# Kernel tuning notes

Hardware: AMD Instinct MI355X
Metric: run time of the kernel (lower is better)

Reference implementation:

```python
import jax, jax.numpy as jnp
import numpy as np

B, N, CS, CZ, H, C, PQ, PV = 1, 512, 384, 128, 12, 16, 4, 8
INF, EPS = 1e5, 1e-8


def _quat_to_rot(q):
    # q: [..., 4] unit quaternion -> [..., 3, 3] rotation matrix
    w, x, y, z = q[..., 0], q[..., 1], q[..., 2], q[..., 3]
    r0 = jnp.stack([1 - 2 * (y * y + z * z), 2 * (x * y - w * z), 2 * (x * z + w * y)], -1)
    r1 = jnp.stack([2 * (x * y + w * z), 1 - 2 * (x * x + z * z), 2 * (y * z - w * x)], -1)
    r2 = jnp.stack([2 * (x * z - w * y), 2 * (y * z + w * x), 1 - 2 * (x * x + y * y)], -1)
    return jnp.stack([r0, r1, r2], -2)


def setup_inputs() -> dict:
    key = jax.random.key(0)
    ks = jax.random.split(key, 20)
    sc = 0.02
    quat = jax.random.normal(ks[0], (B, N, 4), jnp.float32)
    quat = quat / jnp.linalg.norm(quat, axis=-1, keepdims=True)
    concat_dim = H * (C + PV * 4 + CZ)
    return {
        "s": jax.random.normal(ks[1], (B, N, CS), jnp.float32),
        "z": jax.random.normal(ks[2], (B, N, N, CZ), jnp.float32),
        "rot": _quat_to_rot(quat),
        "trans": jax.random.normal(ks[3], (B, N, 3), jnp.float32),
        "mask": jnp.ones((B, N), jnp.float32),
        "W_q": jax.random.normal(ks[4], (CS, H * C), jnp.float32) * sc,
        "b_q": jnp.zeros((H * C,), jnp.float32),
        "W_kv": jax.random.normal(ks[5], (CS, 2 * H * C), jnp.float32) * sc,
        "b_kv": jnp.zeros((2 * H * C,), jnp.float32),
        "W_qp": jax.random.normal(ks[6], (CS, H * PQ * 3), jnp.float32) * sc,
        "b_qp": jnp.zeros((H * PQ * 3,), jnp.float32),
        "W_kvp": jax.random.normal(ks[7], (CS, H * (PQ + PV) * 3), jnp.float32) * sc,
        "b_kvp": jnp.zeros((H * (PQ + PV) * 3,), jnp.float32),
        "W_b": jax.random.normal(ks[8], (CZ, H), jnp.float32) * sc,
        "b_b": jnp.zeros((H,), jnp.float32),
        "head_weights": jnp.full((H,), 0.541324854612918, jnp.float32),  # softplus^-1(1)
        "W_out": jax.random.normal(ks[9], (concat_dim, CS), jnp.float32) * sc,
        "b_out": jnp.zeros((CS,), jnp.float32),
    }


def reference(s, z, rot, trans, mask, W_q, b_q, W_kv, b_kv, W_qp, b_qp, W_kvp, b_kvp,
              W_b, b_b, head_weights, W_out, b_out):
    # scalar projections
    q = (s @ W_q + b_q).reshape(*s.shape[:-1], H, C)              # [B,N,H,C]
    kv = (s @ W_kv + b_kv).reshape(*s.shape[:-1], H, 2 * C)
    k, v = kv[..., :C], kv[..., C:]                               # [B,N,H,C]

    def to_global_pts(lin, npts):
        # lin: [B,N,H*npts*3]; torch layout: split into thirds -> stack as xyz
        p = jnp.stack(jnp.split(lin, 3, axis=-1), axis=-1)        # [B,N,H*npts,3]
        g = jnp.einsum('bnij,bnpj->bnpi', rot, p) + trans[:, :, None, :]
        return g.reshape(*g.shape[:-2], H, npts, 3)

    q_pts = to_global_pts(s @ W_qp + b_qp, PQ)                    # [B,N,H,PQ,3]
    kv_pts = to_global_pts(s @ W_kvp + b_kvp, PQ + PV)
    k_pts, v_pts = kv_pts[..., :PQ, :], kv_pts[..., PQ:, :]       # [B,N,H,PQ/PV,3]

    # attention logits
    bias = z @ W_b + b_b                                          # [B,N,N,H]
    a = jnp.einsum('bihc,bjhc->bhij', q, k) * np.sqrt(1.0 / (3 * C))
    a = a + np.sqrt(1.0 / 3.0) * jnp.transpose(bias, (0, 3, 1, 2))

    d = q_pts[:, :, None] - k_pts[:, None]                        # [B,N,N,H,PQ,3]
    pt_att = jnp.sum(d * d, axis=-1)                              # [B,N,N,H,PQ]
    hw = jax.nn.softplus(head_weights) * np.sqrt(1.0 / (3 * (PQ * 9.0 / 2)))
    pt_att = jnp.sum(pt_att * hw[None, None, None, :, None], axis=-1) * (-0.5)  # [B,N,N,H]
    a = a + jnp.transpose(pt_att, (0, 3, 1, 2))

    sq_mask = INF * (mask[:, :, None] * mask[:, None, :] - 1.0)   # [B,N,N]
    a = jax.nn.softmax(a + sq_mask[:, None], axis=-1)             # [B,H,N,N]

    # aggregation
    o = jnp.einsum('bhij,bjhc->bihc', a, v).reshape(*s.shape[:-1], H * C)
    o_pt = jnp.einsum('bhij,bjhpc->bihpc', a, v_pts)              # [B,N,H,PV,3]
    o_pt = jnp.einsum('bnji,bnhpj->bnhpi', rot, o_pt - trans[:, :, None, None, :])
    o_pt_norm = jnp.sqrt(jnp.sum(o_pt ** 2, -1) + EPS).reshape(*s.shape[:-1], H * PV)
    o_pt = o_pt.reshape(*s.shape[:-1], H * PV, 3)
    o_pair = jnp.einsum('bhij,bijc->bihc', a, z).reshape(*s.shape[:-1], H * CZ)

    cat = jnp.concatenate([o, o_pt[..., 0], o_pt[..., 1], o_pt[..., 2], o_pt_norm, o_pair], -1)
    return cat @ W_out + b_out                                    # [B,N,CS]
```

## Files before the change

### kernel.cpp

```cpp
#include <hip/hip_runtime.h>
#include <hip/hip_bf16.h>
#include <math.h>


#define N_    512
#define CS_   384
#define CZ_   128
#define H_    12
#define INF_  100000.0f
#define EPS_  1e-8f

__global__ __launch_bounds__(256) void proj_gemm(
    const float* __restrict__ A,
    const float* __restrict__ W0, const float* __restrict__ b0, float* __restrict__ C0, int N0,
    const float* __restrict__ W1, const float* __restrict__ b1, float* __restrict__ C1, int N1,
    const float* __restrict__ W2, const float* __restrict__ b2, float* __restrict__ C2, int N2,
    const float* __restrict__ W3, const float* __restrict__ b3, float* __restrict__ C3, int N3)
{
    const float* W; const float* bias; float* C; int Nt;
    switch (blockIdx.z) {
        case 0:  W = W0; bias = b0; C = C0; Nt = N0; break;
        case 1:  W = W1; bias = b1; C = C1; Nt = N1; break;
        case 2:  W = W2; bias = b2; C = C2; Nt = N2; break;
        default: W = W3; bias = b3; C = C3; Nt = N3; break;
    }
    const int n0 = blockIdx.y * 64;
    if (n0 >= Nt) return;
    const int m0 = blockIdx.x * 64;

    __shared__ float As[16 * 68];
    __shared__ float Bs[16 * 68];
    const int t  = threadIdx.x;
    const int tm = t & 15;
    const int tn = t >> 4;

    float acc[4][4];
    #pragma unroll
    for (int r = 0; r < 4; ++r)
        #pragma unroll
        for (int c = 0; c < 4; ++c) acc[r][c] = 0.f;

    for (int k0 = 0; k0 < CS_; k0 += 16) {
        {
            int m = t >> 2, kb = (t & 3) * 4;
            float4 a4 = *(const float4*)(A + (size_t)(m0 + m) * CS_ + k0 + kb);
            As[(kb + 0) * 68 + m] = a4.x;
            As[(kb + 1) * 68 + m] = a4.y;
            As[(kb + 2) * 68 + m] = a4.z;
            As[(kb + 3) * 68 + m] = a4.w;
        }
        {
            int kk = t >> 4, n = (t & 15) * 4;
            int gn = n0 + n;
            const float* wr = W + (size_t)(k0 + kk) * Nt;
            float4 b4;
            b4.x = (gn + 0 < Nt) ? wr[gn + 0] : 0.f;
            b4.y = (gn + 1 < Nt) ? wr[gn + 1] : 0.f;
            b4.z = (gn + 2 < Nt) ? wr[gn + 2] : 0.f;
            b4.w = (gn + 3 < Nt) ? wr[gn + 3] : 0.f;
            *(float4*)(Bs + kk * 68 + n) = b4;
        }
        __syncthreads();
        #pragma unroll
        for (int kk = 0; kk < 16; ++kk) {
            float4 a4 = *(const float4*)(As + kk * 68 + tm * 4);
            float4 b4 = *(const float4*)(Bs + kk * 68 + tn * 4);
            float am[4] = {a4.x, a4.y, a4.z, a4.w};
            float bn[4] = {b4.x, b4.y, b4.z, b4.w};
            #pragma unroll
            for (int r = 0; r < 4; ++r)
                #pragma unroll
                for (int c = 0; c < 4; ++c)
                    acc[r][c] = fmaf(am[r], bn[c], acc[r][c]);
        }
        __syncthreads();
    }
    #pragma unroll
    for (int r = 0; r < 4; ++r) {
        int gm = m0 + tm * 4 + r;
        int gn = n0 + tn * 4;
        float* cr = C + (size_t)gm * Nt;
        #pragma unroll
        for (int c = 0; c < 4; ++c)
            if (gn + c < Nt) cr[gn + c] = acc[r][c] + bias[gn + c];
    }
}

__global__ __launch_bounds__(256) void gemm_ksplit(
    const float* __restrict__ A, const float* __restrict__ W,
    float* __restrict__ P)
{
    const int kc = blockIdx.z;
    const int m0 = blockIdx.x * 64;
    const int n0 = blockIdx.y * 64;

    __shared__ float As[16 * 68];
    __shared__ float Bs[16 * 68];
    const int t  = threadIdx.x;
    const int tm = t & 15;
    const int tn = t >> 4;

    float acc[4][4];
    #pragma unroll
    for (int r = 0; r < 4; ++r)
        #pragma unroll
        for (int c = 0; c < 4; ++c) acc[r][c] = 0.f;

    const int kbeg = kc * 192;
    for (int k0 = kbeg; k0 < kbeg + 192; k0 += 16) {
        {
            int m = t >> 2, kb = (t & 3) * 4;
            float4 a4 = *(const float4*)(A + (size_t)(m0 + m) * 2112 + k0 + kb);
            As[(kb + 0) * 68 + m] = a4.x;
            As[(kb + 1) * 68 + m] = a4.y;
            As[(kb + 2) * 68 + m] = a4.z;
            As[(kb + 3) * 68 + m] = a4.w;
        }
        {
            int kk = t >> 4, n = (t & 15) * 4;
            float4 b4 = *(const float4*)(W + (size_t)(k0 + kk) * 384 + n0 + n);
            *(float4*)(Bs + kk * 68 + n) = b4;
        }
        __syncthreads();
        #pragma unroll
        for (int kk = 0; kk < 16; ++kk) {
            float4 a4 = *(const float4*)(As + kk * 68 + tm * 4);
            float4 b4 = *(const float4*)(Bs + kk * 68 + tn * 4);
            float am[4] = {a4.x, a4.y, a4.z, a4.w};
            float bn[4] = {b4.x, b4.y, b4.z, b4.w};
            #pragma unroll
            for (int r = 0; r < 4; ++r)
                #pragma unroll
                for (int c = 0; c < 4; ++c)
                    acc[r][c] = fmaf(am[r], bn[c], acc[r][c]);
        }
        __syncthreads();
    }
    float* Pk = P + (size_t)kc * (512 * 384);
    #pragma unroll
    for (int r = 0; r < 4; ++r) {
        int gm = m0 + tm * 4 + r;
        *(float4*)(Pk + (size_t)gm * 384 + n0 + tn * 4) =
            make_float4(acc[r][0], acc[r][1], acc[r][2], acc[r][3]);
    }
}

__global__ __launch_bounds__(256) void reduce_out(
    const float* __restrict__ P, const float* __restrict__ bias,
    float* __restrict__ out)
{
    int idx = blockIdx.x * 256 + threadIdx.x;
    const float4* b4 = (const float4*)bias;
    float4 s = b4[idx % 96];
    const float4* P4 = (const float4*)P;
    #pragma unroll
    for (int g = 0; g < 11; ++g) {
        float4 v = P4[(size_t)g * 49152 + idx];
        s.x += v.x; s.y += v.y; s.z += v.z; s.w += v.w;
    }
    ((float4*)out)[idx] = s;
}

__global__ __launch_bounds__(192) void prep_points(
    const float* __restrict__ lqp, const float* __restrict__ lkvp,
    const float* __restrict__ rot, const float* __restrict__ trans,
    const float* __restrict__ kvb,
    float* __restrict__ qp, float* __restrict__ kp,
    float* __restrict__ vT, float* __restrict__ vpT)
{
    const int n = blockIdx.x;
    const int t = threadIdx.x;
    const float* R = rot   + n * 9;
    const float* T = trans + n * 3;

    if (t < 48) {
        float p0 = lqp[n * 144 + t];
        float p1 = lqp[n * 144 + 48 + t];
        float p2 = lqp[n * 144 + 96 + t];
        float* d = qp + n * 144 + t * 3;
        d[0] = R[0]*p0 + R[1]*p1 + R[2]*p2 + T[0];
        d[1] = R[3]*p0 + R[4]*p1 + R[5]*p2 + T[1];
        d[2] = R[6]*p0 + R[7]*p1 + R[8]*p2 + T[2];
    } else {
        int jj = t - 48;
        float p0 = lkvp[n * 432 + jj];
        float p1 = lkvp[n * 432 + 144 + jj];
        float p2 = lkvp[n * 432 + 288 + jj];
        float g0 = R[0]*p0 + R[1]*p1 + R[2]*p2 + T[0];
        float g1 = R[3]*p0 + R[4]*p1 + R[5]*p2 + T[1];
        float g2 = R[6]*p0 + R[7]*p1 + R[8]*p2 + T[2];
        int h = jj / 12, idx = jj % 12;
        if (idx < 4) {
            float* d = kp + n * 144 + (h * 4 + idx) * 3;
            d[0] = g0; d[1] = g1; d[2] = g2;
        } else {
            int r = (idx - 4) * 3;
            vpT[(size_t)(h * 24 + r + 0) * N_ + n] = g0;
            vpT[(size_t)(h * 24 + r + 1) * N_ + n] = g1;
            vpT[(size_t)(h * 24 + r + 2) * N_ + n] = g2;
        }
    }
    vT[(size_t)t * N_ + n] = kvb[(size_t)n * 384 + (t >> 4) * 32 + 16 + (t & 15)];
}

__global__ __launch_bounds__(256) void ipa_core(
    const float* __restrict__ z,   const float* __restrict__ q,
    const float* __restrict__ kvb, const float* __restrict__ qp,
    const float* __restrict__ kp,  const float* __restrict__ vT,
    const float* __restrict__ vpT, const float* __restrict__ Wb,
    const float* __restrict__ bb,  const float* __restrict__ hwraw,
    const float* __restrict__ mask,const float* __restrict__ rot,
    const float* __restrict__ trans, float* __restrict__ cat)
{
    __shared__ float a_s[12 * 516];
    __shared__ float pb[8 * 6 * 132];

    const int i = blockIdx.x;
    const int t = threadIdx.x;

    const float sc_qk = 0.14433756729740643f;
    const float sc_b  = 0.5773502691896258f;
    const float sc_hw = 0.13608276348795434f;

    const float mi = mask[i];
    float hw12[12], bb12[12];
    #pragma unroll
    for (int h = 0; h < 12; ++h) {
        float x = hwraw[h];
        hw12[h] = ((x > 20.f) ? x : log1pf(__expf(x))) * sc_hw;
        bb12[h] = bb[h];
    }

    const float4* qv  = (const float4*)(q  + (size_t)i * 192);
    const float4* qpv = (const float4*)(qp + (size_t)i * 144);

    for (int jj = 0; jj < 2; ++jj) {
        const int j = t + jj * 256;
        float bias[12];
        #pragma unroll
        for (int h = 0; h < 12; ++h) bias[h] = bb12[h];

        const float4* zr = (const float4*)z + ((size_t)i * N_ + j) * 32;
        #pragma unroll 16
        for (int c4 = 0; c4 < 32; ++c4) {
            float4 z4 = zr[c4];
            float zc[4] = {z4.x, z4.y, z4.z, z4.w};
            #pragma unroll
            for (int cc = 0; cc < 4; ++cc) {
                #pragma unroll
                for (int h = 0; h < 12; ++h)
                    bias[h] = fmaf(zc[cc], Wb[(c4 * 4 + cc) * 12 + h], bias[h]);
            }
        }

        const float mt = INF_ * (mi * mask[j] - 1.f);
        const float4* kr  = (const float4*)(kvb + (size_t)j * 384);
        const float4* kpr = (const float4*)(kp  + (size_t)j * 144);
        #pragma unroll
        for (int h = 0; h < 12; ++h) {
            float qk = 0.f;
            #pragma unroll
            for (int c4 = 0; c4 < 4; ++c4) {
                float4 qh = qv[h * 4 + c4];
                float4 kh = kr[h * 8 + c4];
                qk = fmaf(qh.x, kh.x, qk);
                qk = fmaf(qh.y, kh.y, qk);
                qk = fmaf(qh.z, kh.z, qk);
                qk = fmaf(qh.w, kh.w, qk);
            }
            float pt = 0.f;
            #pragma unroll
            for (int r = 0; r < 3; ++r) {
                float4 qh = qpv[h * 3 + r];
                float4 kh = kpr[h * 3 + r];
                float d0 = qh.x - kh.x, d1 = qh.y - kh.y;
                float d2 = qh.z - kh.z, d3 = qh.w - kh.w;
                pt = fmaf(d0, d0, pt); pt = fmaf(d1, d1, pt);
                pt = fmaf(d2, d2, pt); pt = fmaf(d3, d3, pt);
            }
            a_s[h * 516 + j] = fmaf(qk, sc_qk,
                               fmaf(bias[h], sc_b,
                               fmaf(-0.5f * hw12[h], pt, mt)));
        }
    }
    __syncthreads();

    {
        const int w = t >> 6, lane = t & 63;
        #pragma unroll
        for (int hh = 0; hh < 3; ++hh) {
            const int h = w + hh * 4;
            float* row = a_s + h * 516;
            float4 v0 = *(float4*)(row + lane * 8);
            float4 v1 = *(float4*)(row + lane * 8 + 4);
            float m = fmaxf(fmaxf(fmaxf(v0.x, v0.y), fmaxf(v0.z, v0.w)),
                            fmaxf(fmaxf(v1.x, v1.y), fmaxf(v1.z, v1.w)));
            #pragma unroll
            for (int off = 32; off > 0; off >>= 1)
                m = fmaxf(m, __shfl_xor(m, off));
            v0.x = __expf(v0.x - m); v0.y = __expf(v0.y - m);
            v0.z = __expf(v0.z - m); v0.w = __expf(v0.w - m);
            v1.x = __expf(v1.x - m); v1.y = __expf(v1.y - m);
            v1.z = __expf(v1.z - m); v1.w = __expf(v1.w - m);
            float s = v0.x + v0.y + v0.z + v0.w + v1.x + v1.y + v1.z + v1.w;
            #pragma unroll
            for (int off = 32; off > 0; off >>= 1)
                s += __shfl_xor(s, off);
            float inv = 1.f / s;
            v0.x *= inv; v0.y *= inv; v0.z *= inv; v0.w *= inv;
            v1.x *= inv; v1.y *= inv; v1.z *= inv; v1.w *= inv;
            *(float4*)(row + lane * 8)     = v0;
            *(float4*)(row + lane * 8 + 4) = v1;
        }
    }
    __syncthreads();

    float* opt_s = pb;
    #pragma unroll
    for (int rnd = 0; rnd < 2; ++rnd) {
        const int oi = t + rnd * 256;
        if (oi < 480) {
            int h;
            const float* src;
            if (oi < 192) { h = oi >> 4;        src = vT  + (size_t)oi * N_; }
            else          { int pi = oi - 192; h = pi / 24; src = vpT + (size_t)pi * N_; }
            const float4* s4  = (const float4*)src;
            const float4* a4p = (const float4*)(a_s + h * 516);
            float acc = 0.f;
            #pragma unroll 4
            for (int j4 = 0; j4 < 128; ++j4) {
                float4 a4 = a4p[j4];
                float4 v4 = s4[j4];
                acc = fmaf(a4.x, v4.x, acc);
                acc = fmaf(a4.y, v4.y, acc);
                acc = fmaf(a4.z, v4.z, acc);
                acc = fmaf(a4.w, v4.w, acc);
            }
            if (oi < 192) cat[(size_t)i * 2112 + oi] = acc;
            else          opt_s[oi - 192] = acc;
        }
    }
    __syncthreads();

    if (t < 96) {
        const float* R = rot   + i * 9;
        const float* T = trans + i * 3;
        float g0 = opt_s[t * 3 + 0] - T[0];
        float g1 = opt_s[t * 3 + 1] - T[1];
        float g2 = opt_s[t * 3 + 2] - T[2];
        float x  = R[0]*g0 + R[3]*g1 + R[6]*g2;
        float y  = R[1]*g0 + R[4]*g1 + R[7]*g2;
        float zz = R[2]*g0 + R[5]*g1 + R[8]*g2;
        float nrm = sqrtf(x*x + y*y + zz*zz + EPS_);
        float* cr = cat + (size_t)i * 2112;
        cr[192 + t] = x;
        cr[288 + t] = y;
        cr[384 + t] = zz;
        cr[480 + t] = nrm;
    }
    __syncthreads();

    {
        const int c4 = t & 31;
        const int jg = t >> 5;
        float4 acc[12];
        #pragma unroll
        for (int h = 0; h < 12; ++h) acc[h] = make_float4(0.f, 0.f, 0.f, 0.f);

        const float4* zr = (const float4*)z + (size_t)i * (N_ * 32) + c4;
        for (int j4b = 0; j4b < 16; ++j4b) {
            const int jb = jg * 64 + j4b * 4;
            float4 zv[4];
            #pragma unroll
            for (int u = 0; u < 4; ++u) zv[u] = zr[(size_t)(jb + u) * 32];
            #pragma unroll
            for (int h = 0; h < 12; ++h) {
                float4 a4 = *(const float4*)(a_s + h * 516 + jb);
                acc[h].x = fmaf(a4.x, zv[0].x, acc[h].x);
                acc[h].y = fmaf(a4.x, zv[0].y, acc[h].y);
                acc[h].z = fmaf(a4.x, zv[0].z, acc[h].z);
                acc[h].w = fmaf(a4.x, zv[0].w, acc[h].w);
                acc[h].x = fmaf(a4.y, zv[1].x, acc[h].x);
                acc[h].y = fmaf(a4.y, zv[1].y, acc[h].y);
                acc[h].z = fmaf(a4.y, zv[1].z, acc[h].z);
                acc[h].w = fmaf(a4.y, zv[1].w, acc[h].w);
                acc[h].x = fmaf(a4.z, zv[2].x, acc[h].x);
                acc[h].y = fmaf(a4.z, zv[2].y, acc[h].y);
                acc[h].z = fmaf(a4.z, zv[2].z, acc[h].z);
                acc[h].w = fmaf(a4.z, zv[2].w, acc[h].w);
                acc[h].x = fmaf(a4.w, zv[3].x, acc[h].x);
                acc[h].y = fmaf(a4.w, zv[3].y, acc[h].y);
                acc[h].z = fmaf(a4.w, zv[3].z, acc[h].z);
                acc[h].w = fmaf(a4.w, zv[3].w, acc[h].w);
            }
        }

        #pragma unroll
        for (int half = 0; half < 2; ++half) {
            __syncthreads();
            #pragma unroll
            for (int hh = 0; hh < 6; ++hh)
                *(float4*)(pb + (size_t)(jg * 6 + hh) * 132 + c4 * 4) = acc[half * 6 + hh];
            __syncthreads();
            #pragma unroll
            for (int k = 0; k < 3; ++k) {
                const int idx = t + k * 256;
                const int hh = idx >> 7, c = idx & 127;
                float s = 0.f;
                #pragma unroll
                for (int g = 0; g < 8; ++g)
                    s += pb[(size_t)(g * 6 + hh) * 132 + c];
                cat[(size_t)i * 2112 + 576 + half * 768 + idx] = s;
            }
        }
    }
}

extern "C" void kernel_launch(void* const* d_in, const int* in_sizes, int n_in,
                              void* d_out, int out_size, void* d_ws, size_t ws_size,
                              hipStream_t stream)
{
    const float* s     = (const float*)d_in[0];
    const float* z     = (const float*)d_in[1];
    const float* rot   = (const float*)d_in[2];
    const float* trans = (const float*)d_in[3];
    const float* mask  = (const float*)d_in[4];
    const float* W_q   = (const float*)d_in[5];
    const float* b_q   = (const float*)d_in[6];
    const float* W_kv  = (const float*)d_in[7];
    const float* b_kv  = (const float*)d_in[8];
    const float* W_qp  = (const float*)d_in[9];
    const float* b_qp  = (const float*)d_in[10];
    const float* W_kvp = (const float*)d_in[11];
    const float* b_kvp = (const float*)d_in[12];
    const float* W_b   = (const float*)d_in[13];
    const float* b_b   = (const float*)d_in[14];
    const float* hw    = (const float*)d_in[15];
    const float* W_out = (const float*)d_in[16];
    const float* b_out = (const float*)d_in[17];
    float* out = (float*)d_out;
    float* ws  = (float*)d_ws;

    float* q     = ws;
    float* kvb   = q     + 512 * 192;
    float* lqp   = kvb   + 512 * 384;
    float* lkvp  = lqp   + 512 * 144;
    float* qp    = lkvp  + 512 * 432;
    float* kp    = qp    + 512 * 144;
    float* vT    = kp    + 512 * 144;
    float* vpT   = vT    + 192 * 512;
    float* cat   = vpT   + 288 * 512;
    float* gpart = cat   + 512 * 2112;

    proj_gemm<<<dim3(8, 7, 4), 256, 0, stream>>>(
        s,
        W_q,   b_q,   q,    192,
        W_kv,  b_kv,  kvb,  384,
        W_qp,  b_qp,  lqp,  144,
        W_kvp, b_kvp, lkvp, 432);
    prep_points<<<512, 192, 0, stream>>>(lqp, lkvp, rot, trans, kvb, qp, kp, vT, vpT);
    ipa_core<<<512, 256, 0, stream>>>(z, q, kvb, qp, kp, vT, vpT,
                                      W_b, b_b, hw, mask, rot, trans, cat);
    gemm_ksplit<<<dim3(8, 6, 11), 256, 0, stream>>>(cat, W_out, gpart);
    reduce_out<<<192, 256, 0, stream>>>(gpart, b_out, out);
}
```

Before: 406.2 us.

## Stage z tiles in LDS, split heads across waves, row-major value layout

The pair-bias computation now loads 64-row tiles of z into shared memory with coalesced float4 loads. Each wave computes 3 heads for 64 keys instead of every thread computing all 12 heads for two keys, which cuts register pressure and per-thread Wb traffic. Values and value-points are written into a combined row-major buffer, and aggregation reads them as float2 per thread, so two outputs are accumulated per thread. The workspace is also reorganized so gpart aliases the early buffers. The cost is 8 extra syncs per block, a larger LDS footprint, and q/k values re-read per wave.

```diff
diff --git a/kernel.cpp b/kernel.cpp
--- a/kernel.cpp
+++ b/kernel.cpp
@@ -166,7 +166,7 @@
     const float* __restrict__ rot, const float* __restrict__ trans,
     const float* __restrict__ kvb,
     float* __restrict__ qp, float* __restrict__ kp,
-    float* __restrict__ vT, float* __restrict__ vpT)
+    float* __restrict__ vcat)
 {
     const int n = blockIdx.x;
     const int t = threadIdx.x;
@@ -194,62 +194,72 @@
             float* d = kp + n * 144 + (h * 4 + idx) * 3;
             d[0] = g0; d[1] = g1; d[2] = g2;
         } else {
-            int r = (idx - 4) * 3;
-            vpT[(size_t)(h * 24 + r + 0) * N_ + n] = g0;
-            vpT[(size_t)(h * 24 + r + 1) * N_ + n] = g1;
-            vpT[(size_t)(h * 24 + r + 2) * N_ + n] = g2;
-        }
-    }
-    vT[(size_t)t * N_ + n] = kvb[(size_t)n * 384 + (t >> 4) * 32 + 16 + (t & 15)];
+            float* d = vcat + (size_t)n * 512 + 192 + h * 24 + (idx - 4) * 3;
+            d[0] = g0; d[1] = g1; d[2] = g2;
+        }
+    }
+    vcat[(size_t)n * 512 + t] = kvb[(size_t)n * 384 + (t >> 4) * 32 + 16 + (t & 15)];
 }
 
 __global__ __launch_bounds__(256) void ipa_core(
     const float* __restrict__ z,   const float* __restrict__ q,
     const float* __restrict__ kvb, const float* __restrict__ qp,
-    const float* __restrict__ kp,  const float* __restrict__ vT,
-    const float* __restrict__ vpT, const float* __restrict__ Wb,
-    const float* __restrict__ bb,  const float* __restrict__ hwraw,
-    const float* __restrict__ mask,const float* __restrict__ rot,
-    const float* __restrict__ trans, float* __restrict__ cat)
-{
-    __shared__ float a_s[12 * 516];
-    __shared__ float pb[8 * 6 * 132];
-
-    const int i = blockIdx.x;
-    const int t = threadIdx.x;
+    const float* __restrict__ kp,  const float* __restrict__ vcat,
+    const float* __restrict__ Wb,  const float* __restrict__ bb,
+    const float* __restrict__ hwraw, const float* __restrict__ mask,
+    const float* __restrict__ rot, const float* __restrict__ trans,
+    float* __restrict__ cat)
+{
+    __shared__ float4 a_s4[1548];
+    __shared__ float4 pb4[2112];
+    float* a_s = (float*)a_s4;
+    float* pb  = (float*)pb4;
+
+    const int i    = blockIdx.x;
+    const int t    = threadIdx.x;
+    const int lane = t & 63;
 
     const float sc_qk = 0.14433756729740643f;
     const float sc_b  = 0.5773502691896258f;
     const float sc_hw = 0.13608276348795434f;
 
     const float mi = mask[i];
-    float hw12[12], bb12[12];
-    #pragma unroll
-    for (int h = 0; h < 12; ++h) {
-        float x = hwraw[h];
-        hw12[h] = ((x > 20.f) ? x : log1pf(__expf(x))) * sc_hw;
-        bb12[h] = bb[h];
-    }
+
+    const int h0 = __builtin_amdgcn_readfirstlane((t >> 6) * 3);
+    const float bbA = bb[h0],     bbB = bb[h0 + 1],     bbC = bb[h0 + 2];
+    float xA = hwraw[h0], xB = hwraw[h0 + 1], xC = hwraw[h0 + 2];
+    const float hwA = ((xA > 20.f) ? xA : log1pf(__expf(xA))) * sc_hw;
+    const float hwB = ((xB > 20.f) ? xB : log1pf(__expf(xB))) * sc_hw;
+    const float hwC = ((xC > 20.f) ? xC : log1pf(__expf(xC))) * sc_hw;
 
     const float4* qv  = (const float4*)(q  + (size_t)i * 192);
     const float4* qpv = (const float4*)(qp + (size_t)i * 144);
 
-    for (int jj = 0; jj < 2; ++jj) {
-        const int j = t + jj * 256;
-        float bias[12];
-        #pragma unroll
-        for (int h = 0; h < 12; ++h) bias[h] = bb12[h];
-
-        const float4* zr = (const float4*)z + ((size_t)i * N_ + j) * 32;
-        #pragma unroll 16
+    float* ztile = pb;
+    for (int tile = 0; tile < 8; ++tile) {
+        const int jb = tile * 64;
+        const float4* zsrc = (const float4*)z + ((size_t)i * N_ + jb) * 32;
+        #pragma unroll
+        for (int k2 = 0; k2 < 8; ++k2) {
+            int idx = t + k2 * 256;
+            int rr = idx >> 5, c4 = idx & 31;
+            *(float4*)(ztile + rr * 132 + c4 * 4) = zsrc[(size_t)rr * 32 + c4];
+        }
+        __syncthreads();
+
+        const int j = jb + lane;
+        float b0 = bbA, b1 = bbB, b2 = bbC;
+        const float4* zrow = (const float4*)(ztile + lane * 132);
+        #pragma unroll 8
         for (int c4 = 0; c4 < 32; ++c4) {
-            float4 z4 = zr[c4];
+            float4 z4 = zrow[c4];
             float zc[4] = {z4.x, z4.y, z4.z, z4.w};
             #pragma unroll
             for (int cc = 0; cc < 4; ++cc) {
-                #pragma unroll
-                for (int h = 0; h < 12; ++h)
-                    bias[h] = fmaf(zc[cc], Wb[(c4 * 4 + cc) * 12 + h], bias[h]);
+                const int c = c4 * 4 + cc;
+                b0 = fmaf(zc[cc], Wb[c * 12 + h0    ], b0);
+                b1 = fmaf(zc[cc], Wb[c * 12 + h0 + 1], b1);
+                b2 = fmaf(zc[cc], Wb[c * 12 + h0 + 2], b2);
             }
         }
 
@@ -257,7 +267,8 @@
         const float4* kr  = (const float4*)(kvb + (size_t)j * 384);
         const float4* kpr = (const float4*)(kp  + (size_t)j * 144);
         #pragma unroll
-        for (int h = 0; h < 12; ++h) {
+        for (int hh = 0; hh < 3; ++hh) {
+            const int h = h0 + hh;
             float qk = 0.f;
             #pragma unroll
             for (int c4 = 0; c4 < 4; ++c4) {
@@ -278,15 +289,17 @@
                 pt = fmaf(d0, d0, pt); pt = fmaf(d1, d1, pt);
                 pt = fmaf(d2, d2, pt); pt = fmaf(d3, d3, pt);
             }
+            float bsum = (hh == 0) ? b0 : (hh == 1) ? b1 : b2;
+            float hwv  = (hh == 0) ? hwA : (hh == 1) ? hwB : hwC;
             a_s[h * 516 + j] = fmaf(qk, sc_qk,
-                               fmaf(bias[h], sc_b,
-                               fmaf(-0.5f * hw12[h], pt, mt)));
-        }
-    }
-    __syncthreads();
+                               fmaf(bsum, sc_b,
+                               fmaf(-0.5f * hwv, pt, mt)));
+        }
+        __syncthreads();
+    }
 
     {
-        const int w = t >> 6, lane = t & 63;
+        const int w = t >> 6;
         #pragma unroll
         for (int hh = 0; hh < 3; ++hh) {
             const int h = w + hh * 4;
@@ -316,28 +329,24 @@
     __syncthreads();
 
     float* opt_s = pb;
-    #pragma unroll
-    for (int rnd = 0; rnd < 2; ++rnd) {
-        const int oi = t + rnd * 256;
-        if (oi < 480) {
-            int h;
-            const float* src;
-            if (oi < 192) { h = oi >> 4;        src = vT  + (size_t)oi * N_; }
-            else          { int pi = oi - 192; h = pi / 24; src = vpT + (size_t)pi * N_; }
-            const float4* s4  = (const float4*)src;
-            const float4* a4p = (const float4*)(a_s + h * 516);
-            float acc = 0.f;
-            #pragma unroll 4
-            for (int j4 = 0; j4 < 128; ++j4) {
-                float4 a4 = a4p[j4];
-                float4 v4 = s4[j4];
-                acc = fmaf(a4.x, v4.x, acc);
-                acc = fmaf(a4.y, v4.y, acc);
-                acc = fmaf(a4.z, v4.z, acc);
-                acc = fmaf(a4.w, v4.w, acc);
-            }
-            if (oi < 192) cat[(size_t)i * 2112 + oi] = acc;
-            else          opt_s[oi - 192] = acc;
+    if (t < 240) {
+        const int o0 = 2 * t;
+        const int h  = (o0 < 192) ? (o0 >> 4) : ((o0 - 192) / 24);
+        const float2* vrow = (const float2*)vcat + t;
+        float accx = 0.f, accy = 0.f;
+        #pragma unroll 4
+        for (int j = 0; j < 512; ++j) {
+            float2 v2 = vrow[(size_t)j * 256];
+            float aj  = a_s[h * 516 + j];
+            accx = fmaf(aj, v2.x, accx);
+            accy = fmaf(aj, v2.y, accy);
+        }
+        if (o0 < 192) {
+            cat[(size_t)i * 2112 + o0]     = accx;
+            cat[(size_t)i * 2112 + o0 + 1] = accy;
+        } else {
+            opt_s[o0 - 192] = accx;
+            opt_s[o0 - 191] = accy;
         }
     }
     __syncthreads();
@@ -441,16 +450,15 @@
     float* out = (float*)d_out;
     float* ws  = (float*)d_ws;
 
+    float* gpart = ws;
+    float* cat   = ws + 2162688;
     float* q     = ws;
-    float* kvb   = q     + 512 * 192;
-    float* lqp   = kvb   + 512 * 384;
-    float* lkvp  = lqp   + 512 * 144;
-    float* qp    = lkvp  + 512 * 432;
-    float* kp    = qp    + 512 * 144;
-    float* vT    = kp    + 512 * 144;
-    float* vpT   = vT    + 192 * 512;
-    float* cat   = vpT   + 288 * 512;
-    float* gpart = cat   + 512 * 2112;
+    float* kvb   = q    + 98304;
+    float* lqp   = kvb  + 196608;
+    float* lkvp  = lqp  + 73728;
+    float* qp    = lkvp + 221184;
+    float* kp    = qp   + 73728;
+    float* vcat  = kp   + 73728;
 
     proj_gemm<<<dim3(8, 7, 4), 256, 0, stream>>>(
         s,
@@ -458,8 +466,8 @@
         W_kv,  b_kv,  kvb,  384,
         W_qp,  b_qp,  lqp,  144,
         W_kvp, b_kvp, lkvp, 432);
-    prep_points<<<512, 192, 0, stream>>>(lqp, lkvp, rot, trans, kvb, qp, kp, vT, vpT);
-    ipa_core<<<512, 256, 0, stream>>>(z, q, kvb, qp, kp, vT, vpT,
+    prep_points<<<512, 192, 0, stream>>>(lqp, lkvp, rot, trans, kvb, qp, kp, vcat);
+    ipa_core<<<512, 256, 0, stream>>>(z, q, kvb, qp, kp, vcat,
                                       W_b, b_b, hw, mask, rot, trans, cat);
     gemm_ksplit<<<dim3(8, 6, 11), 256, 0, stream>>>(cat, W_out, gpart);
     reduce_out<<<192, 256, 0, stream>>>(gpart, b_out, out);
```

Measured after the change: 387.5 us. 4.6% less time.
